# Kernel optimization log

Measured on AMD Instinct MI355X. Metric: run time of the kernel, lower is better.

## Reference

```python
import jax, jax.numpy as jnp
import numpy as np

K, S, P = 3, 2, 2  # kernel_size, stride, padding (dilation=1)


def _unfold(xp, k, s, oh, ow):
    """Extract k*k strided patches from a padded array.

    xp: (..., Hp, Wp) -> (..., k*k, oh, ow), window-position ordering (kh, kw)
    matching torch.nn.Unfold (channel-major handled by caller).
    """
    return jnp.stack(
        [xp[..., i:i + s * (oh - 1) + 1:s, j:j + s * (ow - 1) + 1:s]
         for i in range(K) for j in range(K)],
        axis=-3,
    )


def setup_inputs() -> dict:
    key = jax.random.key(0)
    x = jax.random.normal(key, (8, 256, 128, 128), dtype=jnp.float32)
    return {"x": x}


def reference(x):
    b, c, h, w = x.shape
    oh = (h - K + 2 * P) // S + 1
    ow = (w - K + 2 * P) // S + 1

    # channel-wise L2 norm, computed BEFORE unfolding (padding contributes 0 either way)
    n = jnp.sqrt(jnp.sum(x * x, axis=1))            # (b, h, w)
    n_pad = jnp.pad(n, ((0, 0), (P, P), (P, P)))
    n_patch = _unfold(n_pad, K, S, oh, ow)          # (b, k*k, oh, ow)
    # weighting_fn = softmax over the k*k window positions (torch dim=1 of unfolded norm)
    wts = jax.nn.softmax(n_patch, axis=1)           # (b, k*k, oh, ow)

    x_pad = jnp.pad(x, ((0, 0), (0, 0), (P, P), (P, P)))
    x_patch = _unfold(x_pad, K, S, oh, ow)          # (b, c, k*k, oh, ow)

    # weighted sum over window positions
    return jnp.sum(wts[:, None] * x_patch, axis=2)  # (b, c, oh, ow)
```

## Files before the change

kernel.cpp:

```cpp
#include <hip/hip_runtime.h>
#include <math.h>

#define BATCH 8
#define CH    256
#define H     128
#define W     128
#define HW    (H * W)
#define OH    65
#define OW    65
#define NPIX  (OH * OW)

__global__ __launch_bounds__(256) void norm_kernel(const float4* __restrict__ x4,
                                                   float* __restrict__ nrm) {
    const int b    = blockIdx.x >> 6;
    const int t    = blockIdx.x & 63;
    const int lane = threadIdx.x & 63;
    const int wv   = threadIdx.x >> 6;

    const float4* p = x4 + (size_t)(b * CH + wv * 64) * (HW / 4) + t * 64 + lane;
    float4 a = {0.f, 0.f, 0.f, 0.f};
    #pragma unroll 8
    for (int c = 0; c < 64; ++c) {
        float4 v = p[(size_t)c * (HW / 4)];
        a.x += v.x * v.x; a.y += v.y * v.y;
        a.z += v.z * v.z; a.w += v.w * v.w;
    }
    __shared__ float part[4][256];
    ((float4*)part[wv])[lane] = a;
    __syncthreads();
    float s = part[0][threadIdx.x] + part[1][threadIdx.x]
            + part[2][threadIdx.x] + part[3][threadIdx.x];
    nrm[(size_t)b * HW + t * 256 + threadIdx.x] = sqrtf(s);
}

#define OHT   33
#define K2TPB 512
#define CPW   32

__global__ __launch_bounds__(K2TPB) void pool_kernel(const float* __restrict__ x,
                                                     const float* __restrict__ nrm,
                                                     float* __restrict__ out) {
    const int b    = blockIdx.x & 7;
    const int ohT  = blockIdx.x >> 3;
    const int oh0  = ohT * 2;
    const bool hasB = (oh0 + 1) < OH;
    const int tid  = threadIdx.x;
    const int lane = tid & 63;
    const int wv   = tid >> 6;

    int rowc[5];
    #pragma unroll
    for (int r = 0; r < 5; ++r) {
        int ih = oh0 * 2 - 2 + r;
        rowc[r] = ih < 0 ? 0 : (ih > H - 1 ? H - 1 : ih);
    }

    __shared__ float ns[5][W];
    __shared__ float wls[2 * OH][9];

    for (int id = tid; id < 5 * W; id += K2TPB) {
        int r = id >> 7, col = id & (W - 1);
        ns[r][col] = nrm[(size_t)b * HW + rowc[r] * W + col];
    }
    __syncthreads();

    if (tid < 2 * OH) {
        int ohl = tid >= OH ? 1 : 0;
        int ow  = tid - ohl * OH;
        int oh  = oh0 + ohl;
        if (oh < OH) {
            int iw0 = ow * 2 - 2;
            float nv[9]; bool val[9]; float m = 0.0f;
            #pragma unroll
            for (int kh = 0; kh < 3; ++kh) {
                int ih = oh * 2 + kh - 2;
                bool vh = (unsigned)ih < (unsigned)H;
                int rL = 2 * ohl + kh;
                #pragma unroll
                for (int kw = 0; kw < 3; ++kw) {
                    int iw = iw0 + kw;
                    int k  = kh * 3 + kw;
                    bool v = vh && ((unsigned)iw < (unsigned)W);
                    val[k] = v;
                    nv[k]  = v ? ns[rL][iw] : 0.0f;
                    m = fmaxf(m, nv[k]);
                }
            }
            float denom = 0.0f, wt[9];
            #pragma unroll
            for (int k = 0; k < 9; ++k) {
                float e = __expf(nv[k] - m);
                denom += e;
                wt[k] = val[k] ? e : 0.0f;
            }
            float inv = 1.0f / denom;
            #pragma unroll
            for (int k = 0; k < 9; ++k) wls[tid][k] = wt[k] * inv;
        }
    }
    __syncthreads();

    const float aA0 = wls[lane][2],     aA1 = wls[lane][5],     aA2 = wls[lane][8];
    const float aB0 = wls[lane + 1][0], aC0 = wls[lane + 1][1];
    const float aB1 = wls[lane + 1][3], aC1 = wls[lane + 1][4];
    const float aB2 = wls[lane + 1][6], aC2 = wls[lane + 1][7];
    const float bA0 = wls[OH + lane][2],     bA1 = wls[OH + lane][5],     bA2 = wls[OH + lane][8];
    const float bB0 = wls[OH + lane + 1][0], bC0 = wls[OH + lane + 1][1];
    const float bB1 = wls[OH + lane + 1][3], bC1 = wls[OH + lane + 1][4];
    const float bB2 = wls[OH + lane + 1][6], bC2 = wls[OH + lane + 1][7];

    const float2* xw2 = (const float2*)x + (size_t)(b * CH + wv * CPW) * (HW / 2);
    const int base0 = rowc[0] * (W / 2) + lane;
    const int base1 = rowc[1] * (W / 2) + lane;
    const int base2 = rowc[2] * (W / 2) + lane;
    const int base3 = rowc[3] * (W / 2) + lane;
    const int base4 = rowc[4] * (W / 2) + lane;

    float* ob = out + (size_t)(b * CH + wv * CPW) * NPIX + (size_t)oh0 * OW;
    #pragma unroll 4
    for (int c = 0; c < CPW; ++c) {
        const size_t cb = (size_t)c * (HW / 2);
        float2 v0 = xw2[cb + base0];
        float2 v1 = xw2[cb + base1];
        float2 v2 = xw2[cb + base2];
        float SA = aB0 * v0.x + aC0 * v0.y
                 + aB1 * v1.x + aC1 * v1.y
                 + aB2 * v2.x + aC2 * v2.y;
        float TA = aA0 * v0.x + aA1 * v1.x + aA2 * v2.x;
        float SpA = __shfl_up(SA, 1);
        float resA = (lane == 0) ? TA : TA + SpA;
        float* oc = ob + (size_t)c * NPIX;
        oc[lane] = resA;
        if (lane == 63) oc[64] = SA;
        if (hasB) {
            float2 v3 = xw2[cb + base3];
            float2 v4 = xw2[cb + base4];
            float SB = bB0 * v2.x + bC0 * v2.y
                     + bB1 * v3.x + bC1 * v3.y
                     + bB2 * v4.x + bC2 * v4.y;
            float TB = bA0 * v2.x + bA1 * v3.x + bA2 * v4.x;
            float SpB = __shfl_up(SB, 1);
            float resB = (lane == 0) ? TB : TB + SpB;
            oc[OW + lane] = resB;
            if (lane == 63) oc[OW + 64] = SB;
        }
    }
}

extern "C" void kernel_launch(void* const* d_in, const int* in_sizes, int n_in,
                              void* d_out, int out_size, void* d_ws, size_t ws_size,
                              hipStream_t stream) {
    const float* x = (const float*)d_in[0];
    float* out  = (float*)d_out;
    float* nbuf = (float*)d_ws;

    norm_kernel<<<512, 256, 0, stream>>>((const float4*)x, nbuf);
    pool_kernel<<<BATCH * OHT, K2TPB, 0, stream>>>(x, nbuf, out);
}
```

Before: 224.1 us.

## Use float4 loads with half-wave per channel and split channels across blocks

The pool kernel now has each 32-lane half-wave handle one channel, loading float4 (four input columns) per lane. Each lane computes two output columns, one fully owned and one finished with a shuffled partial from its neighbour. Channels are split into two groups across twice as many 256-thread blocks. The aim is wider memory transactions, fewer load instructions per output, and more blocks to spread across CUs. The cost is extra weight registers and the softmax weights being recomputed in both channel-group blocks.

```diff
diff --git a/kernel.cpp b/kernel.cpp
--- a/kernel.cpp
+++ b/kernel.cpp
@@ -34,19 +34,22 @@
 }
 
 #define OHT   33
-#define K2TPB 512
-#define CPW   32
+#define K2TPB 256
 
 __global__ __launch_bounds__(K2TPB) void pool_kernel(const float* __restrict__ x,
                                                      const float* __restrict__ nrm,
                                                      float* __restrict__ out) {
-    const int b    = blockIdx.x & 7;
-    const int ohT  = blockIdx.x >> 3;
-    const int oh0  = ohT * 2;
+    const int b   = blockIdx.x & 7;
+    const int rem = blockIdx.x >> 3;
+    const int ohT = rem < OHT ? rem : rem - OHT;
+    const int cg  = rem < OHT ? 0 : 1;
+    const int oh0 = ohT * 2;
     const bool hasB = (oh0 + 1) < OH;
     const int tid  = threadIdx.x;
     const int lane = tid & 63;
     const int wv   = tid >> 6;
+    const int j    = lane & 31;
+    const int h    = lane >> 5;
 
     int rowc[5];
     #pragma unroll
@@ -100,49 +103,62 @@
     }
     __syncthreads();
 
-    const float aA0 = wls[lane][2],     aA1 = wls[lane][5],     aA2 = wls[lane][8];
-    const float aB0 = wls[lane + 1][0], aC0 = wls[lane + 1][1];
-    const float aB1 = wls[lane + 1][3], aC1 = wls[lane + 1][4];
-    const float aB2 = wls[lane + 1][6], aC2 = wls[lane + 1][7];
-    const float bA0 = wls[OH + lane][2],     bA1 = wls[OH + lane][5],     bA2 = wls[OH + lane][8];
-    const float bB0 = wls[OH + lane + 1][0], bC0 = wls[OH + lane + 1][1];
-    const float bB1 = wls[OH + lane + 1][3], bC1 = wls[OH + lane + 1][4];
-    const float bB2 = wls[OH + lane + 1][6], bC2 = wls[OH + lane + 1][7];
+    const float tA0 = wls[2*j][2],   tA1 = wls[2*j][5],   tA2 = wls[2*j][8];
+    const float oA0 = wls[2*j+1][0], oA1 = wls[2*j+1][1], oA2 = wls[2*j+1][2];
+    const float oA3 = wls[2*j+1][3], oA4 = wls[2*j+1][4], oA5 = wls[2*j+1][5];
+    const float oA6 = wls[2*j+1][6], oA7 = wls[2*j+1][7], oA8 = wls[2*j+1][8];
+    const float sA0 = wls[2*j+2][0], sA1 = wls[2*j+2][1];
+    const float sA2 = wls[2*j+2][3], sA3 = wls[2*j+2][4];
+    const float sA4 = wls[2*j+2][6], sA5 = wls[2*j+2][7];
+    const float tB0 = wls[OH+2*j][2],   tB1 = wls[OH+2*j][5],   tB2 = wls[OH+2*j][8];
+    const float oB0 = wls[OH+2*j+1][0], oB1 = wls[OH+2*j+1][1], oB2 = wls[OH+2*j+1][2];
+    const float oB3 = wls[OH+2*j+1][3], oB4 = wls[OH+2*j+1][4], oB5 = wls[OH+2*j+1][5];
+    const float oB6 = wls[OH+2*j+1][6], oB7 = wls[OH+2*j+1][7], oB8 = wls[OH+2*j+1][8];
+    const float sB0 = wls[OH+2*j+2][0], sB1 = wls[OH+2*j+2][1];
+    const float sB2 = wls[OH+2*j+2][3], sB3 = wls[OH+2*j+2][4];
+    const float sB4 = wls[OH+2*j+2][6], sB5 = wls[OH+2*j+2][7];
 
-    const float2* xw2 = (const float2*)x + (size_t)(b * CH + wv * CPW) * (HW / 2);
-    const int base0 = rowc[0] * (W / 2) + lane;
-    const int base1 = rowc[1] * (W / 2) + lane;
-    const int base2 = rowc[2] * (W / 2) + lane;
-    const int base3 = rowc[3] * (W / 2) + lane;
-    const int base4 = rowc[4] * (W / 2) + lane;
+    const int cw = cg * 128 + wv * 32;
+    const float* xl = x + (size_t)(b * CH + cw + h) * HW;
+    float*       ol = out + (size_t)(b * CH + cw + h) * NPIX + (size_t)oh0 * OW;
+    int boff[5];
+    #pragma unroll
+    for (int r = 0; r < 5; ++r) boff[r] = rowc[r] * W + 4 * j;
 
-    float* ob = out + (size_t)(b * CH + wv * CPW) * NPIX + (size_t)oh0 * OW;
     #pragma unroll 4
-    for (int c = 0; c < CPW; ++c) {
-        const size_t cb = (size_t)c * (HW / 2);
-        float2 v0 = xw2[cb + base0];
-        float2 v1 = xw2[cb + base1];
-        float2 v2 = xw2[cb + base2];
-        float SA = aB0 * v0.x + aC0 * v0.y
-                 + aB1 * v1.x + aC1 * v1.y
-                 + aB2 * v2.x + aC2 * v2.y;
-        float TA = aA0 * v0.x + aA1 * v1.x + aA2 * v2.x;
+    for (int c = 0; c < 16; ++c) {
+        const float* xc = xl + (size_t)(2 * c) * HW;
+        float4 v0 = *(const float4*)(xc + boff[0]);
+        float4 v1 = *(const float4*)(xc + boff[1]);
+        float4 v2 = *(const float4*)(xc + boff[2]);
+        float4 v3 = *(const float4*)(xc + boff[3]);
+        float4 v4 = *(const float4*)(xc + boff[4]);
+        float* oc = ol + (size_t)(2 * c) * NPIX;
+
+        float ownA = oA0*v0.x + oA1*v0.y + oA2*v0.z
+                   + oA3*v1.x + oA4*v1.y + oA5*v1.z
+                   + oA6*v2.x + oA7*v2.y + oA8*v2.z;
+        float TA = tA0*v0.x + tA1*v1.x + tA2*v2.x;
+        float SA = sA0*v0.z + sA1*v0.w + sA2*v1.z
+                 + sA3*v1.w + sA4*v2.z + sA5*v2.w;
         float SpA = __shfl_up(SA, 1);
-        float resA = (lane == 0) ? TA : TA + SpA;
-        float* oc = ob + (size_t)c * NPIX;
-        oc[lane] = resA;
-        if (lane == 63) oc[64] = SA;
+        float resA = (j == 0) ? TA : TA + SpA;
+        oc[2*j]     = resA;
+        oc[2*j + 1] = ownA;
+        if (j == 31) oc[64] = SA;
+
         if (hasB) {
-            float2 v3 = xw2[cb + base3];
-            float2 v4 = xw2[cb + base4];
-            float SB = bB0 * v2.x + bC0 * v2.y
-                     + bB1 * v3.x + bC1 * v3.y
-                     + bB2 * v4.x + bC2 * v4.y;
-            float TB = bA0 * v2.x + bA1 * v3.x + bA2 * v4.x;
+            float ownB = oB0*v2.x + oB1*v2.y + oB2*v2.z
+                       + oB3*v3.x + oB4*v3.y + oB5*v3.z
+                       + oB6*v4.x + oB7*v4.y + oB8*v4.z;
+            float TB = tB0*v2.x + tB1*v3.x + tB2*v4.x;
+            float SB = sB0*v2.z + sB1*v2.w + sB2*v3.z
+                     + sB3*v3.w + sB4*v4.z + sB5*v4.w;
             float SpB = __shfl_up(SB, 1);
-            float resB = (lane == 0) ? TB : TB + SpB;
-            oc[OW + lane] = resB;
-            if (lane == 63) oc[OW + 64] = SB;
+            float resB = (j == 0) ? TB : TB + SpB;
+            oc[OW + 2*j]     = resB;
+            oc[OW + 2*j + 1] = ownB;
+            if (j == 31) oc[OW + 64] = SB;
         }
     }
 }
@@ -155,5 +171,5 @@
     float* nbuf = (float*)d_ws;
 
     norm_kernel<<<512, 256, 0, stream>>>((const float4*)x, nbuf);
-    pool_kernel<<<BATCH * OHT, K2TPB, 0, stream>>>(x, nbuf, out);
+    pool_kernel<<<BATCH * OHT * 2, K2TPB, 0, stream>>>(x, nbuf, out);
 }
```

Measured after the change: 221.1 us. About the same (-1.4%).
